# Kernel tuning notes

Measured on AMD Instinct MI355X. Metric: run time of the kernel, lower is better.

Reference implementation:

```python
import jax, jax.numpy as jnp
import numpy as np

NF, NX, GROUP_SIZE = 8192, 2048, 64
N_GROUPS = NX // GROUP_SIZE  # pad = 0 since NX % GROUP_SIZE == 0


def setup_inputs() -> dict:
    key = jax.random.key(0)
    k1, k2, k3, k4, k5 = jax.random.split(key, 5)
    x = jax.random.normal(k1, (4, 2048, NX), dtype=jnp.float32)
    packed = jax.random.randint(k2, (NF, NX // 2), 0, 256, dtype=jnp.int32)
    scales = jax.random.uniform(k3, (NF, N_GROUPS), dtype=jnp.float32)
    zeros = jax.random.randint(k4, (NF, N_GROUPS), 0, 16, dtype=jnp.int32)
    bias = jax.random.normal(k5, (NF,), dtype=jnp.float32)
    return {"x": x, "packed": packed, "scales": scales, "zeros": zeros, "bias": bias}


def _dequantize(packed, scales, zeros):
    # packed: [nf, nx//2] bytes, two int4 nibbles per byte (low nibble first)
    low = packed & 15
    high = (packed >> 4) & 15
    # interleave: q[:, 0::2] = low, q[:, 1::2] = high
    q = jnp.stack([low, high], axis=-1).reshape(NF, NX).astype(jnp.float32)
    q = q.reshape(NF, N_GROUPS, GROUP_SIZE)
    W = (q - zeros.astype(jnp.float32)[:, :, None]) * scales[:, :, None]
    return W.reshape(NF, NX)  # [nf, nx]


def reference(x, packed, scales, zeros, bias):
    W = _dequantize(packed, scales, zeros).astype(x.dtype)  # [nf, nx]
    size_out = x.shape[:-1] + (NF,)
    out = jnp.matmul(x.reshape(-1, NX), W.T) + bias  # addmm
    return out.reshape(size_out)
```

## Files before the change

### kernel.cpp

```cpp
#include <hip/hip_runtime.h>
#include <stdint.h>

#define NF 8192
#define NX 2048
#define MROWS 8192
#define NGROUPS 32
#define NTILE 32

typedef unsigned short u16;
typedef __bf16 bf16x8 __attribute__((ext_vector_type(8)));
typedef float f32x16 __attribute__((ext_vector_type(16)));

#define AS1 __attribute__((address_space(1)))
#define AS3 __attribute__((address_space(3)))

__device__ __forceinline__ void glds16(const void* g, void* l) {
    __builtin_amdgcn_global_load_lds((AS1 void*)(uintptr_t)g,
                                     (AS3 void*)(uintptr_t)l, 16, 0, 0);
}

__device__ __forceinline__ u16 f2bf(float f) {
    unsigned u = __float_as_uint(f);
    return (u16)((u + 0x7FFFu + ((u >> 16) & 1u)) >> 16);
}

__global__ void dequant_kernel(const int* __restrict__ packed,
                               const float* __restrict__ scales,
                               const int* __restrict__ zeros,
                               uint32_t* __restrict__ W2) {
    int tid = blockIdx.x * blockDim.x + threadIdx.x;
    int f = tid >> 10;
    int i = tid & 1023;
    int g = f * NGROUPS + (i >> 5);
    int p = packed[tid];
    float s = scales[g];
    float z = (float)zeros[g];
    float w0 = ((float)(p & 15) - z) * s;
    float w1 = ((float)((p >> 4) & 15) - z) * s;
    W2[tid] = (uint32_t)f2bf(w0) | ((uint32_t)f2bf(w1) << 16);
}

__global__ void cvt_kernel(const float4* __restrict__ x, ushort4* __restrict__ y) {
    int i = blockIdx.x * blockDim.x + threadIdx.x;
    float4 v = x[i];
    ushort4 o;
    o.x = f2bf(v.x); o.y = f2bf(v.y); o.z = f2bf(v.z); o.w = f2bf(v.w);
    y[i] = o;
}


#define BAR    __builtin_amdgcn_s_barrier()
#define LGKM0  asm volatile("s_waitcnt lgkmcnt(0)" ::: "memory")
#define VMCNT0 asm volatile("s_waitcnt vmcnt(0)" ::: "memory")
#define FENCE  __builtin_amdgcn_sched_barrier(0)

#define STAGE(unitOff, bufOff, s0, s1, koff) do { \
    glds16((s0) + (koff), dst0 + (unitOff) + (bufOff)); \
    glds16((s1) + (koff), dst1 + (unitOff) + (bufOff)); \
} while (0)

#define LD8(off) (*(const bf16x8*)(smem + (off)))
#define SWZ(K) (((((K)*2) + hi) ^ l7) << 4)

#define RDA(arr, BUF, K) do { \
    arr[0] = LD8((BUF) + aRow +         SWZ(K)); \
    arr[1] = LD8((BUF) + aRow + 4096  + SWZ(K)); \
    arr[2] = LD8((BUF) + aRow + 16384 + SWZ(K)); \
    arr[3] = LD8((BUF) + aRow + 20480 + SWZ(K)); \
} while (0)

#define RDB(arr, BUF, K) do { \
    arr[0] = LD8((BUF) + bRow + 32768 + SWZ(K)); \
    arr[1] = LD8((BUF) + bRow + 49152 + SWZ(K)); \
} while (0)

#define MM(A_, B_) do { \
    _Pragma("unroll") \
    for (int i_ = 0; i_ < 4; ++i_) { \
        acc[i_][0] = __builtin_amdgcn_mfma_f32_32x32x16_bf16(A_[i_], B_[0], acc[i_][0], 0, 0, 0); \
        acc[i_][1] = __builtin_amdgcn_mfma_f32_32x32x16_bf16(A_[i_], B_[1], acc[i_][1], 0, 0, 0); \
    } \
} while (0)

__global__ __launch_bounds__(512, 2)
void gemm_kernel(const u16* __restrict__ A, const u16* __restrict__ B,
                 const float* __restrict__ bias, float* __restrict__ C) {
    __shared__ __align__(16) char smem[131072];

    const int t = threadIdx.x;

    const int bid = blockIdx.x;
    const int swz = (bid & 7) * 128 + (bid >> 3);
    const int by = swz >> 5;
    const int bx = swz & 31;
    const int rowA0 = by * 256;
    const int rowB0 = bx * 256;

    const int tr = t >> 3;
    const int slot = (t & 7) ^ (tr & 7);
    const int s16 = slot * 16;

    const char* Ab = (const char*)A;
    const char* Bb = (const char*)B;
    const char* srcA1_0 = Ab + (size_t)(rowA0 + tr)       * 4096 + s16;
    const char* srcA1_1 = Ab + (size_t)(rowA0 + 128 + tr) * 4096 + s16;
    const char* srcA2_0 = Ab + (size_t)(rowA0 + 64 + tr)  * 4096 + s16;
    const char* srcA2_1 = Ab + (size_t)(rowA0 + 192 + tr) * 4096 + s16;
    const int rb = (tr >> 5) * 64 + (tr & 31);
    const char* srcB2_0 = Bb + (size_t)(rowB0 + rb)       * 4096 + s16;
    const char* srcB2_1 = Bb + (size_t)(rowB0 + 128 + rb) * 4096 + s16;
    const char* srcB1_0 = Bb + (size_t)(rowB0 + 32 + rb)  * 4096 + s16;
    const char* srcB1_1 = Bb + (size_t)(rowB0 + 160 + rb) * 4096 + s16;

    char* dst0 = smem + t * 16;
    char* dst1 = smem + (t + 512) * 16;

    const int lane = t & 63;
    const int wv = t >> 6;
    const int wm = wv >> 2;
    const int wn = wv & 3;
    const int l31 = lane & 31;
    const int hi = lane >> 5;
    const int l7 = lane & 7;
    const int aRow = (wm * 64 + l31) * 128;
    const int bRow = (wn * 32 + l31) * 128;

    f32x16 acc[4][2];
#pragma unroll
    for (int i = 0; i < 4; ++i)
#pragma unroll
        for (int n = 0; n < 2; ++n)
#pragma unroll
            for (int r = 0; r < 16; ++r) acc[i][n][r] = 0.f;

    bf16x8 aA[4], aB[4], bA[2], bB[2];

    STAGE(0,     0, srcA1_0, srcA1_1, 0);
    STAGE(16384, 0, srcA2_0, srcA2_1, 0);
    STAGE(32768, 0, srcB2_0, srcB2_1, 0);
    STAGE(49152, 0, srcB1_0, srcB1_1, 0);
    VMCNT0;
    BAR;
    RDA(aA, 0, 0);
    RDB(bA, 0, 0);

    int kNext = 128;

#pragma unroll 1
    for (int T = 0; T < NTILE; ++T) {
        const int bo = (T & 1) << 16;
        const int so = bo ^ 65536;
        const bool more = (T + 1 < NTILE);

        FENCE; BAR; LGKM0; FENCE;
        RDA(aB, bo, 1);
        RDB(bB, bo, 1);
        if (more) {
            STAGE(0,     so, srcA1_0, srcA1_1, kNext);
            STAGE(16384, so, srcA2_0, srcA2_1, kNext);
            STAGE(32768, so, srcB2_0, srcB2_1, kNext);
        }
        __builtin_amdgcn_s_setprio(1);
        MM(aA, bA);
        __builtin_amdgcn_s_setprio(0);

        FENCE; BAR; LGKM0; FENCE;
        RDA(aA, bo, 2);
        RDB(bA, bo, 2);
        if (more) STAGE(49152, so, srcB1_0, srcB1_1, kNext);
        __builtin_amdgcn_s_setprio(1);
        MM(aB, bB);
        __builtin_amdgcn_s_setprio(0);

        FENCE; BAR; LGKM0; FENCE;
        RDA(aB, bo, 3);
        RDB(bB, bo, 3);
        __builtin_amdgcn_s_setprio(1);
        MM(aA, bA);
        __builtin_amdgcn_s_setprio(0);
        FENCE;
        VMCNT0;

        FENCE; BAR; LGKM0; FENCE;
        if (more) {
            RDA(aA, so, 0);
            RDB(bA, so, 0);
        }
        __builtin_amdgcn_s_setprio(1);
        MM(aB, bB);
        __builtin_amdgcn_s_setprio(0);

        kNext += 128;
    }

    const int col0 = rowB0 + wn * 64 + l31;
    const int row0 = rowA0 + wm * 128 + 4 * hi;
    const float bj0 = bias[col0];
    const float bj1 = bias[col0 + 32];
    float* Cbase = C + col0;
#pragma unroll
    for (int i = 0; i < 4; ++i) {
#pragma unroll
        for (int r = 0; r < 16; ++r) {
            const int row = row0 + i * 32 + (r & 3) + 8 * (r >> 2);
            float* crow = Cbase + (size_t)row * NF;
            __builtin_nontemporal_store(acc[i][0][r] + bj0, crow);
            __builtin_nontemporal_store(acc[i][1][r] + bj1, crow + 32);
        }
    }
}

extern "C" void kernel_launch(void* const* d_in, const int* in_sizes, int n_in,
                              void* d_out, int out_size, void* d_ws, size_t ws_size,
                              hipStream_t stream) {
    const float* x      = (const float*)d_in[0];
    const int* packed   = (const int*)d_in[1];
    const float* scales = (const float*)d_in[2];
    const int* zeros    = (const int*)d_in[3];
    const float* bias   = (const float*)d_in[4];
    float* out = (float*)d_out;

    u16* Wq = (u16*)d_ws;
    u16* Xb = Wq + (size_t)NF * NX;

    dequant_kernel<<<(NF * (NX / 2)) / 256, 256, 0, stream>>>(packed, scales, zeros, (uint32_t*)Wq);
    cvt_kernel<<<(MROWS * NX / 4) / 256, 256, 0, stream>>>((const float4*)x, (ushort4*)Xb);

    gemm_kernel<<<dim3((MROWS / 256) * (NF / 256)), 512, 0, stream>>>(Xb, Wq, bias, out);
}
```

Measured before the change: 315.2 us.

## Shrink GEMM tile to 128x256 with K=64 triple-buffered LDS pipeline

The GEMM block tile drops from 256x256 to 128x256 and the K step from 128 to 64. LDS is restructured into three rotating 24KB buffers, so loads run two stages ahead and are gated with vmcnt(3) instead of a full drain. Smaller LDS and accumulator footprints let launch bounds target more blocks per CU, trading lower per-block data reuse (more global and LDS traffic per FLOP) for more occupancy and latency hiding.

```diff
diff --git a/kernel.cpp b/kernel.cpp
--- a/kernel.cpp
+++ b/kernel.cpp
@@ -5,7 +5,7 @@
 #define NX 2048
 #define MROWS 8192
 #define NGROUPS 32
-#define NTILE 32
+#define NTILE 64
 
 typedef unsigned short u16;
 typedef __bf16 bf16x8 __attribute__((ext_vector_type(8)));
@@ -51,69 +51,55 @@
 
 #define BAR    __builtin_amdgcn_s_barrier()
 #define LGKM0  asm volatile("s_waitcnt lgkmcnt(0)" ::: "memory")
+#define VMCNT3 asm volatile("s_waitcnt vmcnt(3)" ::: "memory")
 #define VMCNT0 asm volatile("s_waitcnt vmcnt(0)" ::: "memory")
 #define FENCE  __builtin_amdgcn_sched_barrier(0)
 
-#define STAGE(unitOff, bufOff, s0, s1, koff) do { \
-    glds16((s0) + (koff), dst0 + (unitOff) + (bufOff)); \
-    glds16((s1) + (koff), dst1 + (unitOff) + (bufOff)); \
+#define LD8(off) (*(const bf16x8*)(smem + (off)))
+
+#define MFMA32(d, va, vb) d = __builtin_amdgcn_mfma_f32_32x32x16_bf16(va, vb, d, 0, 0, 0)
+
+#define RDBANK(aX, bX, BUF, U) do { \
+    aX[0] = LD8((BUF) + aR0 + (U)); \
+    aX[1] = LD8((BUF) + aR1 + (U)); \
+    bX[0] = LD8((BUF) + bR0 + (U)); \
+    bX[1] = LD8((BUF) + bR1 + (U)); \
 } while (0)
 
-#define LD8(off) (*(const bf16x8*)(smem + (off)))
-#define SWZ(K) (((((K)*2) + hi) ^ l7) << 4)
-
-#define RDA(arr, BUF, K) do { \
-    arr[0] = LD8((BUF) + aRow +         SWZ(K)); \
-    arr[1] = LD8((BUF) + aRow + 4096  + SWZ(K)); \
-    arr[2] = LD8((BUF) + aRow + 16384 + SWZ(K)); \
-    arr[3] = LD8((BUF) + aRow + 20480 + SWZ(K)); \
+#define MM2(aX, bX) do { \
+    MFMA32(acc[0][0], aX[0], bX[0]); \
+    MFMA32(acc[0][1], aX[0], bX[1]); \
+    MFMA32(acc[1][0], aX[1], bX[0]); \
+    MFMA32(acc[1][1], aX[1], bX[1]); \
 } while (0)
 
-#define RDB(arr, BUF, K) do { \
-    arr[0] = LD8((BUF) + bRow + 32768 + SWZ(K)); \
-    arr[1] = LD8((BUF) + bRow + 49152 + SWZ(K)); \
+#define STAGE3(BUF, KOFF) do { \
+    glds16(srcA  + (KOFF), smem + (BUF) + t16); \
+    glds16(srcB0 + (KOFF), smem + (BUF) + 8192 + t16); \
+    glds16(srcB1 + (KOFF), smem + (BUF) + 16384 + t16); \
 } while (0)
 
-#define MM(A_, B_) do { \
-    _Pragma("unroll") \
-    for (int i_ = 0; i_ < 4; ++i_) { \
-        acc[i_][0] = __builtin_amdgcn_mfma_f32_32x32x16_bf16(A_[i_], B_[0], acc[i_][0], 0, 0, 0); \
-        acc[i_][1] = __builtin_amdgcn_mfma_f32_32x32x16_bf16(A_[i_], B_[1], acc[i_][1], 0, 0, 0); \
-    } \
-} while (0)
-
-__global__ __launch_bounds__(512, 2)
+__global__ __launch_bounds__(512, 4)
 void gemm_kernel(const u16* __restrict__ A, const u16* __restrict__ B,
                  const float* __restrict__ bias, float* __restrict__ C) {
-    __shared__ __align__(16) char smem[131072];
+    __shared__ __align__(16) char smem[73728];
 
     const int t = threadIdx.x;
 
     const int bid = blockIdx.x;
-    const int swz = (bid & 7) * 128 + (bid >> 3);
+    const int swz = (bid & 7) * 256 + (bid >> 3);
     const int by = swz >> 5;
     const int bx = swz & 31;
-    const int rowA0 = by * 256;
+    const int rowA0 = by * 128;
     const int rowB0 = bx * 256;
 
-    const int tr = t >> 3;
-    const int slot = (t & 7) ^ (tr & 7);
-    const int s16 = slot * 16;
-
-    const char* Ab = (const char*)A;
-    const char* Bb = (const char*)B;
-    const char* srcA1_0 = Ab + (size_t)(rowA0 + tr)       * 4096 + s16;
-    const char* srcA1_1 = Ab + (size_t)(rowA0 + 128 + tr) * 4096 + s16;
-    const char* srcA2_0 = Ab + (size_t)(rowA0 + 64 + tr)  * 4096 + s16;
-    const char* srcA2_1 = Ab + (size_t)(rowA0 + 192 + tr) * 4096 + s16;
-    const int rb = (tr >> 5) * 64 + (tr & 31);
-    const char* srcB2_0 = Bb + (size_t)(rowB0 + rb)       * 4096 + s16;
-    const char* srcB2_1 = Bb + (size_t)(rowB0 + 128 + rb) * 4096 + s16;
-    const char* srcB1_0 = Bb + (size_t)(rowB0 + 32 + rb)  * 4096 + s16;
-    const char* srcB1_1 = Bb + (size_t)(rowB0 + 160 + rb) * 4096 + s16;
-
-    char* dst0 = smem + t * 16;
-    char* dst1 = smem + (t + 512) * 16;
+    const int t16 = t * 16;
+    const int ulog = (t & 7) ^ ((t >> 3) & 7);
+    const int brow = 2 * (t >> 3) + (ulog >> 2);
+    const int ks16 = (ulog & 3) * 16;
+    const char* srcA  = (const char*)A + (size_t)(rowA0 + brow) * 4096 + ks16;
+    const char* srcB0 = (const char*)B + (size_t)(rowB0 + brow) * 4096 + ks16;
+    const char* srcB1 = srcB0 + (size_t)128 * 4096;
 
     const int lane = t & 63;
     const int wv = t >> 6;
@@ -121,85 +107,64 @@
     const int wn = wv & 3;
     const int l31 = lane & 31;
     const int hi = lane >> 5;
-    const int l7 = lane & 7;
-    const int aRow = (wm * 64 + l31) * 128;
-    const int bRow = (wn * 32 + l31) * 128;
+    const int lh = l31 >> 1;
+    const int x7 = lh & 7;
+    const int ux4 = (l31 & 1) * 4;
+    const int u0 = ((ux4 + 0 + hi) ^ x7) * 16;
+    const int u1 = ((ux4 + 2 + hi) ^ x7) * 16;
+    const int aR0 = (wm * 32 + lh) * 128;
+    const int aR1 = aR0 + 16 * 128;
+    const int bR0 = 8192 + (wn * 32 + lh) * 128;
+    const int bR1 = bR0 + 16 * 128;
 
-    f32x16 acc[4][2];
+    f32x16 acc[2][2];
 #pragma unroll
-    for (int i = 0; i < 4; ++i)
+    for (int i = 0; i < 2; ++i)
 #pragma unroll
         for (int n = 0; n < 2; ++n)
 #pragma unroll
             for (int r = 0; r < 16; ++r) acc[i][n][r] = 0.f;
 
-    bf16x8 aA[4], aB[4], bA[2], bB[2];
+    bf16x8 aE[2], bE[2], aO[2], bO[2];
 
-    STAGE(0,     0, srcA1_0, srcA1_1, 0);
-    STAGE(16384, 0, srcA2_0, srcA2_1, 0);
-    STAGE(32768, 0, srcB2_0, srcB2_1, 0);
-    STAGE(49152, 0, srcB1_0, srcB1_1, 0);
-    VMCNT0;
+    STAGE3(0,     0);
+    STAGE3(24576, 64);
+    VMCNT3;
     BAR;
-    RDA(aA, 0, 0);
-    RDB(bA, 0, 0);
+    RDBANK(aE, bE, 0, u0);
 
-    int kNext = 128;
+    int bufC = 0, bufN = 24576, bufT = 49152;
+    int kOff = 128;
 
 #pragma unroll 1
     for (int T = 0; T < NTILE; ++T) {
-        const int bo = (T & 1) << 16;
-        const int so = bo ^ 65536;
-        const bool more = (T + 1 < NTILE);
-
         FENCE; BAR; LGKM0; FENCE;
-        RDA(aB, bo, 1);
-        RDB(bB, bo, 1);
-        if (more) {
-            STAGE(0,     so, srcA1_0, srcA1_1, kNext);
-            STAGE(16384, so, srcA2_0, srcA2_1, kNext);
-            STAGE(32768, so, srcB2_0, srcB2_1, kNext);
-        }
+        RDBANK(aO, bO, bufC, u1);
+        if (T < NTILE - 2) STAGE3(bufT, kOff);
         __builtin_amdgcn_s_setprio(1);
-        MM(aA, bA);
-        __builtin_amdgcn_s_setprio(0);
-
-        FENCE; BAR; LGKM0; FENCE;
-        RDA(aA, bo, 2);
-        RDB(bA, bo, 2);
-        if (more) STAGE(49152, so, srcB1_0, srcB1_1, kNext);
-        __builtin_amdgcn_s_setprio(1);
-        MM(aB, bB);
-        __builtin_amdgcn_s_setprio(0);
-
-        FENCE; BAR; LGKM0; FENCE;
-        RDA(aB, bo, 3);
-        RDB(bB, bo, 3);
-        __builtin_amdgcn_s_setprio(1);
-        MM(aA, bA);
+        MM2(aE, bE);
         __builtin_amdgcn_s_setprio(0);
         FENCE;
-        VMCNT0;
 
-        FENCE; BAR; LGKM0; FENCE;
-        if (more) {
-            RDA(aA, so, 0);
-            RDB(bA, so, 0);
-        }
+        if (T < NTILE - 2) VMCNT3; else VMCNT0;
+        BAR; LGKM0; FENCE;
+        if (T < NTILE - 1) RDBANK(aE, bE, bufN, u0);
         __builtin_amdgcn_s_setprio(1);
-        MM(aB, bB);
+        MM2(aO, bO);
         __builtin_amdgcn_s_setprio(0);
+        FENCE;
 
-        kNext += 128;
+        const int tmp = bufC; bufC = bufN; bufN = bufT; bufT = tmp;
+        kOff += 64;
     }
 
     const int col0 = rowB0 + wn * 64 + l31;
-    const int row0 = rowA0 + wm * 128 + 4 * hi;
+    const int row0 = rowA0 + wm * 64 + 4 * hi;
     const float bj0 = bias[col0];
     const float bj1 = bias[col0 + 32];
     float* Cbase = C + col0;
 #pragma unroll
-    for (int i = 0; i < 4; ++i) {
+    for (int i = 0; i < 2; ++i) {
 #pragma unroll
         for (int r = 0; r < 16; ++r) {
             const int row = row0 + i * 32 + (r & 3) + 8 * (r >> 2);
@@ -226,5 +191,5 @@
     dequant_kernel<<<(NF * (NX / 2)) / 256, 256, 0, stream>>>(packed, scales, zeros, (uint32_t*)Wq);
     cvt_kernel<<<(MROWS * NX / 4) / 256, 256, 0, stream>>>((const float4*)x, (ushort4*)Xb);
 
-    gemm_kernel<<<dim3((MROWS / 256) * (NF / 256)), 512, 0, stream>>>(Xb, Wq, bias, out);
+    gemm_kernel<<<dim3((MROWS / 128) * (NF / 256)), 512, 0, stream>>>(Xb, Wq, bias, out);
 }
```

New measurement: 369.9 us. 1.17x slower.
